# Performance work log

Measured on AMD Instinct MI355X. Metric: run time of the kernel, lower is better.

The kernel has to match this reference:

```python
import jax, jax.numpy as jnp
import numpy as np

EPS = 1e-9


def setup_inputs() -> dict:
    key = jax.random.key(0)
    k1, k2 = jax.random.split(key)
    batch, num_codes, code_dim = 32768, 8192, 256
    features = jax.random.normal(k1, (batch, code_dim), dtype=jnp.float32)
    codebook = jax.random.normal(k2, (num_codes, code_dim), dtype=jnp.float32)
    return {"features": features, "codebook": codebook}


def reference(features, codebook):
    # squared L2 distances: (B, C)
    distances = (
        jnp.sum(features ** 2, axis=1, keepdims=True)
        + jnp.sum(codebook ** 2, axis=1)
        - 2.0 * features @ codebook.T
    )
    closest = jnp.argmin(distances, axis=1)          # (B,) int32
    quantized = codebook[closest]                    # (B, D) gather

    codebook_loss = jnp.mean((quantized - jax.lax.stop_gradient(features)) ** 2)
    commitment_loss = jnp.mean((features - jax.lax.stop_gradient(quantized)) ** 2)

    soft_probs = jax.nn.softmax(-distances, axis=1)
    per_sample_entropy = -jnp.sum(soft_probs * jnp.log(soft_probs + EPS), axis=1)
    code_entropy = jnp.mean(per_sample_entropy)

    # straight-through estimator
    final_representation = features + jax.lax.stop_gradient(quantized - features)
    return final_representation, codebook_loss, commitment_loss, code_entropy
```

## Files before the change

### kernel.cpp

```cpp
#include <hip/hip_runtime.h>
#include <math.h>


#define DDIM 256
#define BM 128
#define BN 128
#define LOG2E 1.44269504f
#define NEG2L (-2.88539008f)
#define LN2 0.69314718f
#define MARGIN_Y 0.0288539f

typedef short bf16x8 __attribute__((ext_vector_type(8)));
typedef unsigned short ushort8 __attribute__((ext_vector_type(8)));
typedef float f32x4 __attribute__((ext_vector_type(4)));

__device__ __forceinline__ unsigned short f2bf(float f) {
  unsigned u = __float_as_uint(f);
  return (unsigned short)((u + 0x7FFF + ((u >> 16) & 1)) >> 16);
}
__device__ __forceinline__ float bf2f(unsigned short h) {
  return __uint_as_float(((unsigned)h) << 16);
}
__device__ __forceinline__ void gload_lds16(const void* g, void* l) {
  __builtin_amdgcn_global_load_lds(
      (const __attribute__((address_space(1))) void*)g,
      (__attribute__((address_space(3))) void*)l, 16, 0, 0);
}

__global__ void init_kernel(int* flagCount, float* lossAcc, float* hAcc) {
  if (threadIdx.x == 0) { *flagCount = 0; *lossAcc = 0.f; *hAcc = 0.f; }
}

__global__ void cvt_cb_kernel(const float* __restrict__ cb,
                              unsigned short* __restrict__ hi,
                              unsigned short* __restrict__ lo) {
  const size_t base = ((size_t)blockIdx.x * 256 + threadIdx.x) * 8;
  const float4 f0 = *reinterpret_cast<const float4*>(cb + base);
  const float4 f1 = *reinterpret_cast<const float4*>(cb + base + 4);
  float fv[8] = {f0.x, f0.y, f0.z, f0.w, f1.x, f1.y, f1.z, f1.w};
  ushort8 h, l;
  #pragma unroll
  for (int e = 0; e < 8; ++e) {
    unsigned short hh = f2bf(fv[e]);
    h[e] = hh;
    l[e] = f2bf(fv[e] - bf2f(hh));
  }
  *reinterpret_cast<ushort8*>(hi + base) = h;
  *reinterpret_cast<ushort8*>(lo + base) = l;
}

__global__ void cn_kernel(const float* __restrict__ cb, float* __restrict__ cn) {
  const int lane = threadIdx.x & 63;
  const int wave = threadIdx.x >> 6;
  const int c = blockIdx.x * 4 + wave;
  const float4 v = *reinterpret_cast<const float4*>(cb + (size_t)c * DDIM + lane * 4);
  float s = v.x * v.x + v.y * v.y + v.z * v.z + v.w * v.w;
  #pragma unroll
  for (int off = 1; off < 64; off <<= 1) s += __shfl_xor(s, off, 64);
  if (lane == 0) cn[c] = s;
}

__launch_bounds__(256, 1)
__global__ void dist_kernel(const float* __restrict__ feat,
                            const unsigned short* __restrict__ cbhi,
                            const unsigned short* __restrict__ cblo,
                            const float* __restrict__ cn,
                            float* __restrict__ Hrow,
                            int* __restrict__ aminArr,
                            int* __restrict__ flagged,
                            int* __restrict__ flagCount,
                            int C) {
  __shared__ unsigned short sFhi[BM * DDIM];
  __shared__ unsigned short sFlo[BM * DDIM];
  __shared__ unsigned short sChi[BN * 64];
  __shared__ unsigned short sClo[BN * 64];
  const int tid = threadIdx.x;
  const int lane = tid & 63;
  const int w = tid >> 6;
  const int lr = lane & 15;
  const int g = lane >> 4;
  const size_t rowBase = (size_t)blockIdx.x * BM;

  char* sFhiB = (char*)sFhi; char* sFloB = (char*)sFlo;
  char* sChiB = (char*)sChi; char* sCloB = (char*)sClo;

  #pragma unroll 1
  for (int it = 0; it < 16; ++it) {
    int idx8 = tid + it * 256;
    int row = idx8 >> 5;
    int k8 = idx8 & 31;
    const float* fp = feat + (rowBase + row) * DDIM + k8 * 8;
    const float4 f0 = *reinterpret_cast<const float4*>(fp);
    const float4 f1 = *reinterpret_cast<const float4*>(fp + 4);
    float fv[8] = {f0.x, f0.y, f0.z, f0.w, f1.x, f1.y, f1.z, f1.w};
    ushort8 h, l;
    #pragma unroll
    for (int e = 0; e < 8; ++e) {
      unsigned short hh = f2bf(fv[e]);
      h[e] = hh;
      l[e] = f2bf(fv[e] - bf2f(hh));
    }
    int off = (k8 * 16) ^ ((row & 7) << 4);
    *reinterpret_cast<ushort8*>(sFhiB + row * 512 + off) = h;
    *reinterpret_cast<ushort8*>(sFloB + row * 512 + off) = l;
  }

  float dminY[8], dmin2Y[8], mmY[8], ss[8], vv[8];
  int am[8];
  #pragma unroll
  for (int i = 0; i < 8; ++i) {
    dminY[i] = INFINITY; dmin2Y[i] = INFINITY;
    mmY[i] = 1e9f; ss[i] = 0.f; vv[i] = 0.f; am[i] = 0;
  }

  const int nchunk = C / BN;
  #pragma unroll 1
  for (int ch = 0; ch < nchunk; ++ch) {
    const int cBase = ch * BN;
    float cnL[8];
    #pragma unroll
    for (int nt = 0; nt < 8; ++nt)
      cnL[nt] = cn[cBase + nt * 16 + lr] * LOG2E;

    f32x4 acc[2][8];
    #pragma unroll
    for (int mt = 0; mt < 2; ++mt)
      #pragma unroll
      for (int nt = 0; nt < 8; ++nt)
        acc[mt][nt] = (f32x4){0.f, 0.f, 0.f, 0.f};

    #pragma unroll 1
    for (int kt = 0; kt < 4; ++kt) {
      __syncthreads();
      #pragma unroll
      for (int it = 0; it < 4; ++it) {
        int L = w * 4096 + it * 1024 + lane * 16;
        int code = L >> 7;
        int kb = L & 127;
        size_t srcOff = (((size_t)(cBase + code)) << 9) + (size_t)kt * 128 +
                        (kb ^ ((code & 7) << 4));
        gload_lds16((const char*)cbhi + srcOff, sChiB + w * 4096 + it * 1024);
        gload_lds16((const char*)cblo + srcOff, sCloB + w * 4096 + it * 1024);
      }
      __syncthreads();

      #pragma unroll
      for (int ks = 0; ks < 2; ++ks) {
        bf16x8 ahi[2], alo[2];
        #pragma unroll
        for (int mt = 0; mt < 2; ++mt) {
          int row = w * 32 + mt * 16 + lr;
          int off = (kt * 128 + ks * 64 + g * 16) ^ ((row & 7) << 4);
          ahi[mt] = *reinterpret_cast<const bf16x8*>(sFhiB + row * 512 + off);
          alo[mt] = *reinterpret_cast<const bf16x8*>(sFloB + row * 512 + off);
        }
        #pragma unroll
        for (int nt = 0; nt < 8; ++nt) {
          int code = nt * 16 + lr;
          int boff = (ks * 64 + g * 16) ^ ((code & 7) << 4);
          bf16x8 bhi = *reinterpret_cast<const bf16x8*>(sChiB + code * 128 + boff);
          bf16x8 blo = *reinterpret_cast<const bf16x8*>(sCloB + code * 128 + boff);
          #pragma unroll
          for (int mt = 0; mt < 2; ++mt) {
            acc[mt][nt] = __builtin_amdgcn_mfma_f32_16x16x32_bf16(ahi[mt], bhi, acc[mt][nt], 0, 0, 0);
            acc[mt][nt] = __builtin_amdgcn_mfma_f32_16x16x32_bf16(alo[mt], bhi, acc[mt][nt], 0, 0, 0);
            acc[mt][nt] = __builtin_amdgcn_mfma_f32_16x16x32_bf16(ahi[mt], blo, acc[mt][nt], 0, 0, 0);
          }
        }
      }
    }

    #pragma unroll
    for (int mt = 0; mt < 2; ++mt) {
      #pragma unroll
      for (int r = 0; r < 4; ++r) {
        const int s = mt * 4 + r;
        float y[8];
        #pragma unroll
        for (int nt = 0; nt < 8; ++nt)
          y[nt] = fmaf(acc[mt][nt][r], NEG2L, cnL[nt]);
        float m8 = fminf(fminf(fminf(y[0], y[1]), fminf(y[2], y[3])),
                         fminf(fminf(y[4], y[5]), fminf(y[6], y[7])));
        float nm = fminf(mmY[s], m8);
        float scl = __builtin_amdgcn_exp2f(nm - mmY[s]);
        ss[s] *= scl; vv[s] *= scl; mmY[s] = nm;
        #pragma unroll
        for (int nt = 0; nt < 8; ++nt) {
          float e = __builtin_amdgcn_exp2f(nm - y[nt]);
          ss[s] += e;
          vv[s] = fmaf(y[nt], e, vv[s]);
          int cidx = cBase + nt * 16 + lr;
          bool lt = y[nt] < dminY[s];
          dmin2Y[s] = fminf(dmin2Y[s], fmaxf(y[nt], dminY[s]));
          am[s] = lt ? cidx : am[s];
          dminY[s] = fminf(dminY[s], y[nt]);
        }
      }
    }
  }

  #pragma unroll
  for (int i = 0; i < 8; ++i) {
    #pragma unroll
    for (int off = 1; off <= 8; off <<= 1) {
      float od = __shfl_xor(dminY[i], off, 64);
      float od2 = __shfl_xor(dmin2Y[i], off, 64);
      int oa = __shfl_xor(am[i], off, 64);
      float om = __shfl_xor(mmY[i], off, 64);
      float os = __shfl_xor(ss[i], off, 64);
      float ov = __shfl_xor(vv[i], off, 64);
      float hi = fmaxf(dminY[i], od);
      dmin2Y[i] = fminf(fminf(dmin2Y[i], od2), hi);
      am[i] = (od < dminY[i]) ? oa : ((od == dminY[i]) ? (oa < am[i] ? oa : am[i]) : am[i]);
      dminY[i] = fminf(dminY[i], od);
      float nm = fminf(mmY[i], om);
      float sa = __builtin_amdgcn_exp2f(nm - mmY[i]);
      float sb = __builtin_amdgcn_exp2f(nm - om);
      ss[i] = ss[i] * sa + os * sb;
      vv[i] = vv[i] * sa + ov * sb;
      mmY[i] = nm;
    }
    if (lr == 0) {
      size_t row = rowBase + w * 32 + (i >> 2) * 16 + 4 * g + (i & 3);
      Hrow[row] = logf(ss[i]) + LN2 * (vv[i] / ss[i] - mmY[i]);
      aminArr[row] = am[i];
      if (dmin2Y[i] - dminY[i] < MARGIN_Y) {
        int slot = atomicAdd(flagCount, 1);
        flagged[slot] = (int)row;
      }
    }
  }
}

__launch_bounds__(256)
__global__ void refine_kernel(const float* __restrict__ feat,
                              const float* __restrict__ cb,
                              int* __restrict__ aminArr,
                              const int* __restrict__ flagged,
                              const int* __restrict__ flagCount,
                              int C) {
  __shared__ double sRow[DDIM];
  __shared__ double sMin[256];
  __shared__ int sIdx[256];
  const int tid = threadIdx.x;
  const int nf = *flagCount;
  for (int f = blockIdx.x; f < nf; f += gridDim.x) {
    const int row = flagged[f];
    sRow[tid] = (double)feat[(size_t)row * DDIM + tid];
    __syncthreads();
    double lmin = 1e300; int lidx = 0;
    #pragma unroll 1
    for (int c = tid; c < C; c += 256) {
      const float* cp = cb + (size_t)c * DDIM;
      double s0 = 0.0, s1 = 0.0;
      #pragma unroll 4
      for (int d = 0; d < DDIM; d += 8) {
        const float4 a = *reinterpret_cast<const float4*>(cp + d);
        const float4 b = *reinterpret_cast<const float4*>(cp + d + 4);
        double d0 = sRow[d]     - (double)a.x;
        double d1 = sRow[d + 1] - (double)a.y;
        double d2 = sRow[d + 2] - (double)a.z;
        double d3 = sRow[d + 3] - (double)a.w;
        double e0 = sRow[d + 4] - (double)b.x;
        double e1 = sRow[d + 5] - (double)b.y;
        double e2 = sRow[d + 6] - (double)b.z;
        double e3 = sRow[d + 7] - (double)b.w;
        s0 += d0 * d0 + d1 * d1 + d2 * d2 + d3 * d3;
        s1 += e0 * e0 + e1 * e1 + e2 * e2 + e3 * e3;
      }
      const double s = s0 + s1;
      if (s < lmin) { lmin = s; lidx = c; }
    }
    sMin[tid] = lmin; sIdx[tid] = lidx;
    __syncthreads();
    #pragma unroll
    for (int stride = 128; stride > 0; stride >>= 1) {
      if (tid < stride) {
        const double o = sMin[tid + stride]; const int oi = sIdx[tid + stride];
        if (o < sMin[tid] || (o == sMin[tid] && oi < sIdx[tid])) {
          sMin[tid] = o; sIdx[tid] = oi;
        }
      }
      __syncthreads();
    }
    if (tid == 0) aminArr[row] = sIdx[0];
    __syncthreads();
  }
}

__launch_bounds__(256)
__global__ void gather_kernel(const float* __restrict__ feat,
                              const float* __restrict__ cb,
                              const int* __restrict__ aminArr,
                              const float* __restrict__ Hrow,
                              float* __restrict__ out,
                              float* lossAcc, float* hAcc) {
  const int tid = threadIdx.x;
  const int lane = tid & 63;
  const int wave = tid >> 6;
  const size_t base = (size_t)blockIdx.x * 64;
  float lsum = 0.f;
  #pragma unroll 1
  for (int r = wave; r < 64; r += 4) {
    const size_t row = base + r;
    const int q = aminArr[row];
    const float4 cv = *reinterpret_cast<const float4*>(cb + (size_t)q * DDIM + lane * 4);
    const float4 fv = *reinterpret_cast<const float4*>(feat + row * DDIM + lane * 4);
    *reinterpret_cast<float4*>(out + row * DDIM + lane * 4) = cv;
    const float dx = cv.x - fv.x, dy = cv.y - fv.y, dz = cv.z - fv.z, dw = cv.w - fv.w;
    lsum += dx * dx + dy * dy + dz * dz + dw * dw;
  }
  #pragma unroll
  for (int off = 1; off < 64; off <<= 1) lsum += __shfl_xor(lsum, off, 64);
  __shared__ float wsum[4];
  if (lane == 0) wsum[wave] = lsum;
  __syncthreads();
  if (tid == 0) atomicAdd(lossAcc, wsum[0] + wsum[1] + wsum[2] + wsum[3]);
  if (wave == 0) {
    float h = Hrow[base + lane];
    #pragma unroll
    for (int off = 1; off < 64; off <<= 1) h += __shfl_xor(h, off, 64);
    if (lane == 0) atomicAdd(hAcc, h);
  }
}

__global__ void finalize_kernel(const float* lossAcc, const float* hAcc,
                                float* out, size_t M, float invBD, float invB) {
  if (threadIdx.x == 0) {
    float L = *lossAcc * invBD;
    out[M] = L;
    out[M + 1] = L;
    out[M + 2] = *hAcc * invB;
  }
}

extern "C" void kernel_launch(void* const* d_in, const int* in_sizes, int n_in,
                              void* d_out, int out_size, void* d_ws, size_t ws_size,
                              hipStream_t stream) {
  (void)n_in; (void)out_size; (void)ws_size;
  const float* feat = (const float*)d_in[0];
  const float* cb   = (const float*)d_in[1];
  const int B = in_sizes[0] / DDIM;
  const int C = in_sizes[1] / DDIM;
  float* out = (float*)d_out;

  unsigned short* cbhi = (unsigned short*)d_ws;
  unsigned short* cblo = cbhi + (size_t)C * DDIM;
  float* cn      = (float*)(cblo + (size_t)C * DDIM);
  float* Hrow    = cn + C;
  int*   amin    = (int*)(Hrow + B);
  int*   flagged = amin + B;
  int*   flagCount = flagged + B;
  float* lossAcc = (float*)(flagCount + 1);
  float* hAcc    = lossAcc + 1;

  init_kernel<<<1, 64, 0, stream>>>(flagCount, lossAcc, hAcc);
  cvt_cb_kernel<<<(C * DDIM) / (256 * 8), 256, 0, stream>>>(cb, cbhi, cblo);
  cn_kernel<<<C / 4, 256, 0, stream>>>(cb, cn);
  dist_kernel<<<B / BM, 256, 0, stream>>>(feat, cbhi, cblo, cn, Hrow, amin,
                                          flagged, flagCount, C);
  refine_kernel<<<256, 256, 0, stream>>>(feat, cb, amin, flagged, flagCount, C);
  gather_kernel<<<B / 64, 256, 0, stream>>>(feat, cb, amin, Hrow, out, lossAcc, hAcc);
  finalize_kernel<<<1, 64, 0, stream>>>(lossAcc, hAcc, out,
                                        (size_t)B * DDIM,
                                        1.0f / ((float)B * (float)DDIM),
                                        1.0f / (float)B);
}
```

Before: 803.5 us.

## Double-buffer codebook staging and split waves 2x2 over rows and codes

```diff
diff --git a/kernel.cpp b/kernel.cpp
--- a/kernel.cpp
+++ b/kernel.cpp
@@ -9,6 +9,7 @@
 #define NEG2L (-2.88539008f)
 #define LN2 0.69314718f
 #define MARGIN_Y 0.0288539f
+#define SC0 131072
 
 typedef short bf16x8 __attribute__((ext_vector_type(8)));
 typedef unsigned short ushort8 __attribute__((ext_vector_type(8)));
@@ -70,19 +71,53 @@
                             int* __restrict__ flagged,
                             int* __restrict__ flagCount,
                             int C) {
-  __shared__ unsigned short sFhi[BM * DDIM];
-  __shared__ unsigned short sFlo[BM * DDIM];
-  __shared__ unsigned short sChi[BN * 64];
-  __shared__ unsigned short sClo[BN * 64];
+  __shared__ __align__(1024) char smem[163840];
   const int tid = threadIdx.x;
   const int lane = tid & 63;
   const int w = tid >> 6;
+  const int wr = w >> 1;
+  const int wc = w & 1;
   const int lr = lane & 15;
   const int g = lane >> 4;
   const size_t rowBase = (size_t)blockIdx.x * BM;
 
-  char* sFhiB = (char*)sFhi; char* sFloB = (char*)sFlo;
-  char* sChiB = (char*)sChi; char* sCloB = (char*)sClo;
+  const int e = lr & 7;
+  const int Q = ((g ^ (e & 3)) << 4) + ((e >> 2) << 6);
+  const char* baseAe[4]; const char* baseAo[4];
+  #pragma unroll
+  for (int mt = 0; mt < 4; ++mt) {
+    int row = wr * 64 + mt * 16 + lr;
+    baseAe[mt] = smem + row * 1024 + Q;
+    baseAo[mt] = smem + row * 1024 + (Q ^ 64);
+  }
+  const int vB = (((lane & 1) * 4 + g) ^ ((lr >> 1) & 7)) * 16;
+  const char* baseB0 = smem + SC0 + wc * 4096 + (lr >> 1) * 128 + vB;
+  const char* baseB1 = baseB0 + 16384;
+
+  int c_[2], gp_[2];
+  #pragma unroll
+  for (int it = 0; it < 2; ++it) {
+    int L = w * 2048 + it * 1024 + lane * 16;
+    int rowp = L >> 7;
+    int vlog = ((L >> 4) & 7) ^ (rowp & 7);
+    c_[it] = 2 * rowp + (vlog >> 2);
+    gp_[it] = vlog & 3;
+  }
+  const char* pH0 = (const char*)cbhi + c_[0] * 512 + gp_[0] * 16;
+  const char* pH1 = (const char*)cbhi + c_[1] * 512 + gp_[1] * 16;
+  const char* pL0 = (const char*)cblo + c_[0] * 512 + gp_[0] * 16;
+  const char* pL1 = (const char*)cblo + c_[1] * 512 + gp_[1] * 16;
+
+#define STAGE(BUF, ADV) do { \
+    char* d_ = smem + SC0 + (BUF) * 16384 + w * 2048; \
+    gload_lds16(pH0, d_); \
+    gload_lds16(pH1, d_ + 1024); \
+    gload_lds16(pL0, d_ + 8192); \
+    gload_lds16(pL1, d_ + 9216); \
+    pH0 += (ADV); pH1 += (ADV); pL0 += (ADV); pL1 += (ADV); \
+  } while (0)
+
+  STAGE(0, 64);
 
   #pragma unroll 1
   for (int it = 0; it < 16; ++it) {
@@ -95,101 +130,87 @@
     float fv[8] = {f0.x, f0.y, f0.z, f0.w, f1.x, f1.y, f1.z, f1.w};
     ushort8 h, l;
     #pragma unroll
-    for (int e = 0; e < 8; ++e) {
-      unsigned short hh = f2bf(fv[e]);
-      h[e] = hh;
-      l[e] = f2bf(fv[e] - bf2f(hh));
-    }
-    int off = (k8 * 16) ^ ((row & 7) << 4);
-    *reinterpret_cast<ushort8*>(sFhiB + row * 512 + off) = h;
-    *reinterpret_cast<ushort8*>(sFloB + row * 512 + off) = l;
-  }
-
-  float dminY[8], dmin2Y[8], mmY[8], ss[8], vv[8];
-  int am[8];
-  #pragma unroll
-  for (int i = 0; i < 8; ++i) {
+    for (int ee = 0; ee < 8; ++ee) {
+      unsigned short hh = f2bf(fv[ee]);
+      h[ee] = hh;
+      l[ee] = f2bf(fv[ee] - bf2f(hh));
+    }
+    int off = row * 1024 + ((k8 ^ (row & 7)) << 4);
+    *reinterpret_cast<ushort8*>(smem + off) = h;
+    *reinterpret_cast<ushort8*>(smem + off + 512) = l;
+  }
+  __syncthreads();
+
+  float dminY[16], dmin2Y[16], mmY[16], ss[16], vv[16];
+  int am[16];
+  #pragma unroll
+  for (int i = 0; i < 16; ++i) {
     dminY[i] = INFINITY; dmin2Y[i] = INFINITY;
     mmY[i] = 1e9f; ss[i] = 0.f; vv[i] = 0.f; am[i] = 0;
   }
+
+  f32x4 acc[4][4];
+
+#define PHASE(KT) do { \
+    STAGE(((KT) + 1) & 1, ((KT) == 6) ? 65088 : 64); \
+    bf16x8 ah[4], al[4]; \
+    _Pragma("unroll") \
+    for (int mt = 0; mt < 4; ++mt) { \
+      const char* ab_ = (((KT) & 1) ? baseAo[mt] : baseAe[mt]) + ((KT) >> 1) * 128; \
+      ah[mt] = *reinterpret_cast<const bf16x8*>(ab_); \
+      al[mt] = *reinterpret_cast<const bf16x8*>(ab_ + 512); \
+    } \
+    _Pragma("unroll") \
+    for (int nt = 0; nt < 4; ++nt) { \
+      const char* bb_ = (((KT) & 1) ? baseB1 : baseB0) + nt * 1024; \
+      bf16x8 bh = *reinterpret_cast<const bf16x8*>(bb_); \
+      bf16x8 bl = *reinterpret_cast<const bf16x8*>(bb_ + 8192); \
+      _Pragma("unroll") \
+      for (int mt = 0; mt < 4; ++mt) { \
+        acc[mt][nt] = __builtin_amdgcn_mfma_f32_16x16x32_bf16(ah[mt], bh, acc[mt][nt], 0, 0, 0); \
+        acc[mt][nt] = __builtin_amdgcn_mfma_f32_16x16x32_bf16(al[mt], bh, acc[mt][nt], 0, 0, 0); \
+        acc[mt][nt] = __builtin_amdgcn_mfma_f32_16x16x32_bf16(ah[mt], bl, acc[mt][nt], 0, 0, 0); \
+      } \
+    } \
+    __syncthreads(); \
+  } while (0)
 
   const int nchunk = C / BN;
   #pragma unroll 1
   for (int ch = 0; ch < nchunk; ++ch) {
     const int cBase = ch * BN;
-    float cnL[8];
-    #pragma unroll
-    for (int nt = 0; nt < 8; ++nt)
-      cnL[nt] = cn[cBase + nt * 16 + lr] * LOG2E;
-
-    f32x4 acc[2][8];
-    #pragma unroll
-    for (int mt = 0; mt < 2; ++mt)
+    float cnL[4];
+    #pragma unroll
+    for (int nt = 0; nt < 4; ++nt)
+      cnL[nt] = cn[cBase + wc * 64 + nt * 16 + lr] * LOG2E;
+    #pragma unroll
+    for (int mt = 0; mt < 4; ++mt)
       #pragma unroll
-      for (int nt = 0; nt < 8; ++nt)
+      for (int nt = 0; nt < 4; ++nt)
         acc[mt][nt] = (f32x4){0.f, 0.f, 0.f, 0.f};
 
-    #pragma unroll 1
-    for (int kt = 0; kt < 4; ++kt) {
-      __syncthreads();
-      #pragma unroll
-      for (int it = 0; it < 4; ++it) {
-        int L = w * 4096 + it * 1024 + lane * 16;
-        int code = L >> 7;
-        int kb = L & 127;
-        size_t srcOff = (((size_t)(cBase + code)) << 9) + (size_t)kt * 128 +
-                        (kb ^ ((code & 7) << 4));
-        gload_lds16((const char*)cbhi + srcOff, sChiB + w * 4096 + it * 1024);
-        gload_lds16((const char*)cblo + srcOff, sCloB + w * 4096 + it * 1024);
-      }
-      __syncthreads();
-
-      #pragma unroll
-      for (int ks = 0; ks < 2; ++ks) {
-        bf16x8 ahi[2], alo[2];
-        #pragma unroll
-        for (int mt = 0; mt < 2; ++mt) {
-          int row = w * 32 + mt * 16 + lr;
-          int off = (kt * 128 + ks * 64 + g * 16) ^ ((row & 7) << 4);
-          ahi[mt] = *reinterpret_cast<const bf16x8*>(sFhiB + row * 512 + off);
-          alo[mt] = *reinterpret_cast<const bf16x8*>(sFloB + row * 512 + off);
-        }
-        #pragma unroll
-        for (int nt = 0; nt < 8; ++nt) {
-          int code = nt * 16 + lr;
-          int boff = (ks * 64 + g * 16) ^ ((code & 7) << 4);
-          bf16x8 bhi = *reinterpret_cast<const bf16x8*>(sChiB + code * 128 + boff);
-          bf16x8 blo = *reinterpret_cast<const bf16x8*>(sCloB + code * 128 + boff);
-          #pragma unroll
-          for (int mt = 0; mt < 2; ++mt) {
-            acc[mt][nt] = __builtin_amdgcn_mfma_f32_16x16x32_bf16(ahi[mt], bhi, acc[mt][nt], 0, 0, 0);
-            acc[mt][nt] = __builtin_amdgcn_mfma_f32_16x16x32_bf16(alo[mt], bhi, acc[mt][nt], 0, 0, 0);
-            acc[mt][nt] = __builtin_amdgcn_mfma_f32_16x16x32_bf16(ahi[mt], blo, acc[mt][nt], 0, 0, 0);
-          }
-        }
-      }
-    }
-
-    #pragma unroll
-    for (int mt = 0; mt < 2; ++mt) {
+    PHASE(0); PHASE(1); PHASE(2); PHASE(3);
+    PHASE(4); PHASE(5); PHASE(6); PHASE(7);
+
+    #pragma unroll
+    for (int mt = 0; mt < 4; ++mt) {
       #pragma unroll
       for (int r = 0; r < 4; ++r) {
         const int s = mt * 4 + r;
-        float y[8];
+        float y[4];
         #pragma unroll
-        for (int nt = 0; nt < 8; ++nt)
+        for (int nt = 0; nt < 4; ++nt)
           y[nt] = fmaf(acc[mt][nt][r], NEG2L, cnL[nt]);
-        float m8 = fminf(fminf(fminf(y[0], y[1]), fminf(y[2], y[3])),
-                         fminf(fminf(y[4], y[5]), fminf(y[6], y[7])));
-        float nm = fminf(mmY[s], m8);
+        float m4 = fminf(fminf(y[0], y[1]), fminf(y[2], y[3]));
+        float nm = fminf(mmY[s], m4);
         float scl = __builtin_amdgcn_exp2f(nm - mmY[s]);
         ss[s] *= scl; vv[s] *= scl; mmY[s] = nm;
         #pragma unroll
-        for (int nt = 0; nt < 8; ++nt) {
-          float e = __builtin_amdgcn_exp2f(nm - y[nt]);
-          ss[s] += e;
-          vv[s] = fmaf(y[nt], e, vv[s]);
-          int cidx = cBase + nt * 16 + lr;
+        for (int nt = 0; nt < 4; ++nt) {
+          float ev = __builtin_amdgcn_exp2f(nm - y[nt]);
+          ss[s] += ev;
+          vv[s] = fmaf(y[nt], ev, vv[s]);
+          int cidx = cBase + wc * 64 + nt * 16 + lr;
           bool lt = y[nt] < dminY[s];
           dmin2Y[s] = fminf(dmin2Y[s], fmaxf(y[nt], dminY[s]));
           am[s] = lt ? cidx : am[s];
@@ -200,7 +221,7 @@
   }
 
   #pragma unroll
-  for (int i = 0; i < 8; ++i) {
+  for (int i = 0; i < 16; ++i) {
     #pragma unroll
     for (int off = 1; off <= 8; off <<= 1) {
       float od = __shfl_xor(dminY[i], off, 64);
@@ -221,15 +242,39 @@
       mmY[i] = nm;
     }
     if (lr == 0) {
-      size_t row = rowBase + w * 32 + (i >> 2) * 16 + 4 * g + (i & 3);
-      Hrow[row] = logf(ss[i]) + LN2 * (vv[i] / ss[i] - mmY[i]);
-      aminArr[row] = am[i];
-      if (dmin2Y[i] - dminY[i] < MARGIN_Y) {
-        int slot = atomicAdd(flagCount, 1);
-        flagged[slot] = (int)row;
-      }
-    }
-  }
+      int rowl = wr * 64 + (i >> 2) * 16 + g * 4 + (i & 3);
+      float* mb = reinterpret_cast<float*>(smem) + (size_t)(wc * 128 + rowl) * 8;
+      mb[0] = dminY[i]; mb[1] = dmin2Y[i]; mb[2] = __int_as_float(am[i]);
+      mb[3] = mmY[i];   mb[4] = ss[i];     mb[5] = vv[i];
+    }
+  }
+  __syncthreads();
+
+  if (tid < 128) {
+    const float* a = reinterpret_cast<const float*>(smem) + (size_t)tid * 8;
+    const float* b = a + 128 * 8;
+    float da = a[0], d2a = a[1], ma = a[3], sa_ = a[4], va = a[5];
+    int   aa = __float_as_int(a[2]);
+    float db = b[0], d2b = b[1], mb_ = b[3], sb_ = b[4], vb = b[5];
+    int   ab = __float_as_int(b[2]);
+    float dmin = fminf(da, db);
+    float dmin2 = fminf(fminf(d2a, d2b), fmaxf(da, db));
+    int amF = (da < db) ? aa : ((db < da) ? ab : (aa < ab ? aa : ab));
+    float nm = fminf(ma, mb_);
+    float ea = __builtin_amdgcn_exp2f(nm - ma);
+    float eb = __builtin_amdgcn_exp2f(nm - mb_);
+    float S = sa_ * ea + sb_ * eb;
+    float V = va * ea + vb * eb;
+    size_t row = rowBase + tid;
+    Hrow[row] = logf(S) + LN2 * (V / S - nm);
+    aminArr[row] = amF;
+    if (dmin2 - dmin < MARGIN_Y) {
+      int slot = atomicAdd(flagCount, 1);
+      flagged[slot] = (int)row;
+    }
+  }
+#undef PHASE
+#undef STAGE
 }
 
 __launch_bounds__(256)
```

Measured after the change: 708.1 us. 1.13x faster.
